# Kernel tuning notes

Measured on AMD Instinct MI355X. Metric: run time of the kernel, lower is better.

Reference implementation:

```python
import jax, jax.numpy as jnp
import numpy as np

R_MAX = 6.0
P = 3.0


def _envelope(distance, r_max=R_MAX, p=P):
    d = distance / r_max
    env = (1.0
           - (p + 1.0) * (p + 2.0) / 2.0 * d ** p
           + p * (p + 2.0) * d ** (p + 1.0)
           - p * (p + 1.0) / 2.0 * d ** (p + 2.0))
    return env * (distance < r_max)


def setup_inputs() -> dict:
    key = jax.random.key(0)
    k1, k2, k3, k4, k5 = jax.random.split(key, 5)
    N, K, C, SIZE = 50000, 32, 128, 128
    pair = jax.random.normal(k1, (N, K, C), dtype=jnp.float32)
    pair_update = jax.random.normal(k2, (N, K, SIZE), dtype=jnp.float32)
    neighbours = jax.random.randint(k3, (N, K), 0, N, dtype=jnp.int32)
    pair_mask = jnp.ones((N, K), dtype=bool)
    distance = jax.random.uniform(k4, (N,), dtype=jnp.float32)
    W = jax.random.normal(k5, (C, SIZE), dtype=jnp.float32) / np.sqrt(C)
    return {"pair": pair, "pair_update": pair_update, "neighbours": neighbours,
            "pair_mask": pair_mask, "distance": distance, "W": W}


def reference(pair, pair_update, neighbours, pair_mask, distance, W):
    N, K, _ = pair.shape
    size = W.shape[1]
    # gated message: sigmoid(pair @ W) * pair_update, shape [N, K, size]
    gate = jax.nn.sigmoid(jnp.einsum('nkc,cs->nks', pair, W))
    message = gate * pair_update
    message = jnp.where(pair_mask[..., None], message, 0)
    # polynomial envelope cutoff on per-node distance, broadcast [N,1,1]
    message = message * _envelope(distance)[:, None, None]
    # direction == 'outgoing': scatter-add over neighbour indices
    out = jnp.zeros((N, size), dtype=pair.dtype).at[neighbours].add(message)
    return out
```

## Files before the change

kernel.cpp:

```cpp
#include <hip/hip_runtime.h>
#include <stdint.h>

#define KNBR 32
#define CDIM 128
#define SDIM 128

typedef __bf16 bf16x8 __attribute__((ext_vector_type(8)));
typedef unsigned short ushortx8 __attribute__((ext_vector_type(8)));
typedef float f32x4 __attribute__((ext_vector_type(4)));

__device__ __forceinline__ unsigned short f32_bf16(float f) {
    unsigned int u = __builtin_bit_cast(unsigned int, f);
    u += 0x7FFFu + ((u >> 16) & 1u);
    return (unsigned short)(u >> 16);
}

__device__ __forceinline__ float envelope_fac(float dist, int msk) {
    const float d  = dist * (1.0f / 6.0f);
    const float d3 = d * d * d;
    float env = 1.0f - 10.0f * d3 + 15.0f * d3 * d - 6.0f * d3 * d * d;
    env = (dist < 6.0f) ? env : 0.0f;
    return (msk != 0) ? env : 0.0f;
}


__global__ void k_hist(const int* __restrict__ nbr, int* __restrict__ cnt, int np4) {
    const int i = blockIdx.x * blockDim.x + threadIdx.x;
    if (i < np4) {
        const int4 v = ((const int4*)nbr)[i];
        atomicAdd(&cnt[v.x], 1);
        atomicAdd(&cnt[v.y], 1);
        atomicAdd(&cnt[v.z], 1);
        atomicAdd(&cnt[v.w], 1);
    }
}

__global__ __launch_bounds__(256)
void k_blocksum(const int* __restrict__ cnt, int* __restrict__ bsum, int n) {
    const int t = threadIdx.x;
    const int e0 = blockIdx.x * 1024 + t * 4;
    int s = 0;
    if (e0 + 3 < n) {
        const int4 v = *(const int4*)(cnt + e0);
        s = v.x + v.y + v.z + v.w;
    } else {
        for (int j = 0; j < 4; ++j) if (e0 + j < n) s += cnt[e0 + j];
    }
#pragma unroll
    for (int off = 1; off < 64; off <<= 1) s += __shfl_xor(s, off);
    __shared__ int wt[4];
    if ((t & 63) == 0) wt[t >> 6] = s;
    __syncthreads();
    if (t == 0) bsum[blockIdx.x] = wt[0] + wt[1] + wt[2] + wt[3];
}

__global__ __launch_bounds__(1024)
void k_scanbsum(int* __restrict__ bsum, int nb) {
    __shared__ int lds[1024];
    const int t = threadIdx.x;
    const int own = (t < nb) ? bsum[t] : 0;
    lds[t] = own;
    __syncthreads();
    for (int off = 1; off < 1024; off <<= 1) {
        const int v = (t >= off) ? lds[t - off] : 0;
        __syncthreads();
        lds[t] += v;
        __syncthreads();
    }
    if (t < nb) bsum[t] = lds[t] - own;
}

__global__ __launch_bounds__(256)
void k_finalscan(const int* bsum, int* rowptr, int* cursor, int n) {
    const int t = threadIdx.x;
    const int e0 = blockIdx.x * 1024 + t * 4;
    int v[4] = {0, 0, 0, 0};
    if (e0 + 3 < n) {
        const int4 q = *(const int4*)(cursor + e0);
        v[0] = q.x; v[1] = q.y; v[2] = q.z; v[3] = q.w;
    } else {
        for (int j = 0; j < 4; ++j) if (e0 + j < n) v[j] = cursor[e0 + j];
    }
    const int s0 = v[0], s1 = s0 + v[1], s2 = s1 + v[2], s3 = s2 + v[3];
    const int lane = t & 63, wid = t >> 6;
    int incl = s3;
#pragma unroll
    for (int off = 1; off < 64; off <<= 1) {
        const int u = __shfl_up(incl, off);
        if (lane >= off) incl += u;
    }
    __shared__ int wt[4];
    if (lane == 63) wt[wid] = incl;
    __syncthreads();
    int wpre = 0;
    for (int w = 0; w < wid; ++w) wpre += wt[w];
    const int texcl = (incl - s3) + wpre + bsum[blockIdx.x];
    const int si[4] = {s0, s1, s2, s3};
    const int se[4] = {0, s0, s1, s2};
#pragma unroll
    for (int j = 0; j < 4; ++j) {
        const int e = e0 + j;
        if (e < n) {
            rowptr[1 + e] = texcl + si[j];
            cursor[e]     = texcl + se[j];
        }
    }
    if (blockIdx.x == 0 && t == 0) rowptr[0] = 0;
}

__global__ void k_scatter(const int* __restrict__ nbr, int* __restrict__ cursor,
                          int* __restrict__ elist, int np4) {
    const int i = blockIdx.x * blockDim.x + threadIdx.x;
    if (i < np4) {
        const int4 v = ((const int4*)nbr)[i];
        const int e0 = i * 4;
        elist[atomicAdd(&cursor[v.x], 1)] = e0;
        elist[atomicAdd(&cursor[v.y], 1)] = e0 + 1;
        elist[atomicAdd(&cursor[v.z], 1)] = e0 + 2;
        elist[atomicAdd(&cursor[v.w], 1)] = e0 + 3;
    }
}

__global__ __launch_bounds__(256, 3)
void k_gather(const float* __restrict__ pair,
              const float* __restrict__ pair_update,
              const int*   __restrict__ pair_mask,
              const float* __restrict__ distance,
              const float* __restrict__ W,
              const int*   __restrict__ rowptr,
              const int*   __restrict__ elist,
              float* __restrict__ out,
              int nnodes)
{
    __shared__ uint4 wlds[2048];
    const int tid  = threadIdx.x;
    const int lane = tid & 63;
    const int r16  = lane & 15;
    const int g    = lane >> 4;

    for (int e = tid; e < 2048; e += 256) {
        const int el = e & 63, kk = (e >> 6) & 3, ct = e >> 8;
        const int eg = el >> 4, er = el & 15;
        ushortx8 wb;
#pragma unroll
        for (int j = 0; j < 8; ++j)
            wb[j] = f32_bf16(W[(kk * 32 + eg * 8 + j) * SDIM + ct * 16 + er]);
        wlds[e] = __builtin_bit_cast(uint4, wb);
    }
    __syncthreads();

    const int wave   = (int)((blockIdx.x * blockDim.x + tid) >> 6);
    const int nwaves = (int)((gridDim.x * blockDim.x) >> 6);

    int wbase = 0;

    for (int n0 = wave; n0 < nnodes; n0 += nwaves) {
        const int n    = __builtin_amdgcn_readfirstlane(n0);
        const int base = rowptr[n];
        const int deg  = rowptr[n + 1] - base;
        const int ntile = (deg + 15) >> 4;

        float accs[8];
#pragma unroll
        for (int ct = 0; ct < 8; ++ct) accs[ct] = 0.0f;

        for (int t = 0; t < ntile; ++t) {
            const int slotA = t * 16 + r16;
            const int idxA  = base + ((slotA < deg) ? slotA : 0);
            const int emA   = elist[idxA];
            const float dA  = distance[emA >> 5];
            const int   mA  = pair_mask[emA];
            float facA = envelope_fac(dA, mA);
            facA = (slotA < deg) ? facA : 0.0f;

            int em_e[4]; float fac_e[4];
#pragma unroll
            for (int reg = 0; reg < 4; ++reg) {
                em_e[reg]  = __shfl(emA,  g * 4 + reg);
                fac_e[reg] = __shfl(facA, g * 4 + reg);
            }

            float puv[4][8];
#pragma unroll
            for (int reg = 0; reg < 4; ++reg) {
                const float* pub = pair_update + (size_t)em_e[reg] * SDIM + r16;
#pragma unroll
                for (int ct = 0; ct < 8; ++ct) puv[reg][ct] = pub[ct * 16];
            }

            const float* arow = pair + (size_t)emA * CDIM + g * 8;
            bf16x8 afrag[4];
#pragma unroll
            for (int kk = 0; kk < 4; ++kk) {
                const f32x4 v0 = *(const f32x4*)(arow + kk * 32);
                const f32x4 v1 = *(const f32x4*)(arow + kk * 32 + 4);
                ushortx8 ab;
#pragma unroll
                for (int j = 0; j < 4; ++j) ab[j] = f32_bf16(v0[j]);
#pragma unroll
                for (int j = 0; j < 4; ++j) ab[4 + j] = f32_bf16(v1[j]);
                afrag[kk] = __builtin_bit_cast(bf16x8, ab);
            }

            f32x4 acc[8];
#pragma unroll
            for (int ct = 0; ct < 8; ++ct) acc[ct] = (f32x4){0.f, 0.f, 0.f, 0.f};
            asm volatile("" : "+v"(wbase));
#pragma unroll
            for (int kk = 0; kk < 4; ++kk) {
#pragma unroll
                for (int ct = 0; ct < 8; ++ct) {
                    const uint4* wp = (const uint4*)((const char*)wlds + wbase)
                                      + (ct * 4 + kk) * 64 + lane;
                    const bf16x8 b = __builtin_bit_cast(bf16x8, *wp);
                    acc[ct] = __builtin_amdgcn_mfma_f32_16x16x32_bf16(
                        afrag[kk], b, acc[ct], 0, 0, 0);
                }
            }

#pragma unroll
            for (int reg = 0; reg < 4; ++reg) {
#pragma unroll
                for (int ct = 0; ct < 8; ++ct) {
                    const float logit = acc[ct][reg];
                    const float gate  = __builtin_amdgcn_rcpf(1.0f + __expf(-logit));
                    accs[ct] += gate * puv[reg][ct] * fac_e[reg];
                }
            }
        }

#pragma unroll
        for (int ct = 0; ct < 8; ++ct) {
            float v = accs[ct];
            v += __shfl_xor(v, 16);
            v += __shfl_xor(v, 32);
            accs[ct] = v;
        }
        float* orow = out + (size_t)n * SDIM;
        orow[lane]      = accs[g];
        orow[lane + 64] = accs[4 + g];
    }
}

__global__ __launch_bounds__(256, 2)
void orb_message_atomic(const float* __restrict__ pair,
                        const float* __restrict__ pair_update,
                        const int*   __restrict__ neighbours,
                        const int*   __restrict__ pair_mask,
                        const float* __restrict__ distance,
                        const float* __restrict__ W,
                        float* __restrict__ out,
                        int ntiles)
{
    const int lane = threadIdx.x & 63;
    const int r16  = lane & 15;
    const int g    = lane >> 4;
    const int wave   = (int)((blockIdx.x * blockDim.x + threadIdx.x) >> 6);
    const int nwaves = (int)((gridDim.x * blockDim.x) >> 6);

    bf16x8 wfrag[8][4];
#pragma unroll
    for (int ct = 0; ct < 8; ++ct)
#pragma unroll
        for (int kk = 0; kk < 4; ++kk) {
            ushortx8 wb;
#pragma unroll
            for (int j = 0; j < 8; ++j)
                wb[j] = f32_bf16(W[(kk * 32 + g * 8 + j) * SDIM + ct * 16 + r16]);
            wfrag[ct][kk] = __builtin_bit_cast(bf16x8, wb);
        }

    for (int t = wave; t < ntiles; t += nwaves) {
        const int p0 = t * 16;
        bf16x8 afrag[4];
        const float* arow = pair + (size_t)(p0 + r16) * CDIM + g * 8;
#pragma unroll
        for (int kk = 0; kk < 4; ++kk) {
            const f32x4 v0 = *(const f32x4*)(arow + kk * 32);
            const f32x4 v1 = *(const f32x4*)(arow + kk * 32 + 4);
            ushortx8 ab;
#pragma unroll
            for (int j = 0; j < 4; ++j) ab[j] = f32_bf16(v0[j]);
#pragma unroll
            for (int j = 0; j < 4; ++j) ab[4 + j] = f32_bf16(v1[j]);
            afrag[kk] = __builtin_bit_cast(bf16x8, ab);
        }
        f32x4 acc[8];
#pragma unroll
        for (int ct = 0; ct < 8; ++ct) acc[ct] = (f32x4){0.f, 0.f, 0.f, 0.f};
#pragma unroll
        for (int kk = 0; kk < 4; ++kk)
#pragma unroll
            for (int ct = 0; ct < 8; ++ct)
                acc[ct] = __builtin_amdgcn_mfma_f32_16x16x32_bf16(
                    afrag[kk], wfrag[ct][kk], acc[ct], 0, 0, 0);
#pragma unroll
        for (int reg = 0; reg < 4; ++reg) {
            const int p   = p0 + g * 4 + reg;
            const int tgt = neighbours[p];
            const float fac = envelope_fac(distance[p >> 5], pair_mask[p]);
            const float* pu = pair_update + (size_t)p * SDIM + r16;
            float* op = out + (size_t)tgt * SDIM + r16;
#pragma unroll
            for (int ct = 0; ct < 8; ++ct) {
                const float logit = acc[ct][reg];
                const float gate  = __builtin_amdgcn_rcpf(1.0f + __expf(-logit));
                unsafeAtomicAdd(op + ct * 16, gate * pu[ct * 16] * fac);
            }
        }
    }
}

extern "C" void kernel_launch(void* const* d_in, const int* in_sizes, int n_in,
                              void* d_out, int out_size, void* d_ws, size_t ws_size,
                              hipStream_t stream) {
    const float* pair        = (const float*)d_in[0];
    const float* pair_update = (const float*)d_in[1];
    const int*   neighbours  = (const int*)d_in[2];
    const int*   pair_mask   = (const int*)d_in[3];
    const float* distance    = (const float*)d_in[4];
    const float* W           = (const float*)d_in[5];
    float* out = (float*)d_out;

    const int N      = in_sizes[4];
    const int npairs = N * KNBR;
    const int nb     = (N + 1023) / 1024;

    const size_t need = ((size_t)N + (size_t)(N + 1) + (size_t)npairs + (size_t)nb)
                        * sizeof(int);
    if (ws_size < need || (npairs & 3) != 0 || nb > 1024) {
        hipMemsetAsync(d_out, 0, (size_t)out_size * sizeof(float), stream);
        orb_message_atomic<<<dim3(512), dim3(256), 0, stream>>>(
            pair, pair_update, neighbours, pair_mask, distance, W, out, npairs / 16);
        return;
    }

    int* cursor = (int*)d_ws;
    int* rowptr = cursor + N;
    int* elist  = rowptr + (N + 1);
    int* bsum   = elist + npairs;

    const int np4 = npairs / 4;

    hipMemsetAsync(cursor, 0, (size_t)N * sizeof(int), stream);
    k_hist     <<<dim3((np4 + 255) / 256), dim3(256),  0, stream>>>(neighbours, cursor, np4);
    k_blocksum <<<dim3(nb),                dim3(256),  0, stream>>>(cursor, bsum, N);
    k_scanbsum <<<dim3(1),                 dim3(1024), 0, stream>>>(bsum, nb);
    k_finalscan<<<dim3(nb),                dim3(256),  0, stream>>>(bsum, rowptr, cursor, N);
    k_scatter  <<<dim3((np4 + 255) / 256), dim3(256),  0, stream>>>(neighbours, cursor, elist, np4);
    k_gather   <<<dim3(4096),              dim3(256),  0, stream>>>(
        pair, pair_update, pair_mask, distance, W, rowptr, elist, out, N);
}
```

Baseline: 550.6 us.

## Precompute envelope factors in scatter and prefetch next tile's edge entries

The scatter pass now computes each pair's masked envelope factor and stores it with the edge id as an int2 in the edge list. This removes the dependent distance and mask loads from the gather kernel's inner loop. The gather loop also loads the next tile's edge entry one iteration early and issues the pair-row loads before the pair_update loads, to shorten the dependent load chain. The cost is a wider edge list, which doubles its write and read traffic, plus a few extra registers in the gather kernel.

```diff
diff --git a/kernel.cpp b/kernel.cpp
--- a/kernel.cpp
+++ b/kernel.cpp
@@ -108,27 +108,33 @@
     if (blockIdx.x == 0 && t == 0) rowptr[0] = 0;
 }
 
-__global__ void k_scatter(const int* __restrict__ nbr, int* __restrict__ cursor,
-                          int* __restrict__ elist, int np4) {
+__global__ void k_scatter(const int* __restrict__ nbr,
+                          const int* __restrict__ pair_mask,
+                          const float* __restrict__ distance,
+                          int* __restrict__ cursor,
+                          int2* __restrict__ elist2, int np4) {
     const int i = blockIdx.x * blockDim.x + threadIdx.x;
     if (i < np4) {
         const int4 v = ((const int4*)nbr)[i];
+        const int4 m = ((const int4*)pair_mask)[i];
         const int e0 = i * 4;
-        elist[atomicAdd(&cursor[v.x], 1)] = e0;
-        elist[atomicAdd(&cursor[v.y], 1)] = e0 + 1;
-        elist[atomicAdd(&cursor[v.z], 1)] = e0 + 2;
-        elist[atomicAdd(&cursor[v.w], 1)] = e0 + 3;
+        const float f0 = envelope_fac(distance[(e0 + 0) >> 5], m.x);
+        const float f1 = envelope_fac(distance[(e0 + 1) >> 5], m.y);
+        const float f2 = envelope_fac(distance[(e0 + 2) >> 5], m.z);
+        const float f3 = envelope_fac(distance[(e0 + 3) >> 5], m.w);
+        elist2[atomicAdd(&cursor[v.x], 1)] = make_int2(e0,     __builtin_bit_cast(int, f0));
+        elist2[atomicAdd(&cursor[v.y], 1)] = make_int2(e0 + 1, __builtin_bit_cast(int, f1));
+        elist2[atomicAdd(&cursor[v.z], 1)] = make_int2(e0 + 2, __builtin_bit_cast(int, f2));
+        elist2[atomicAdd(&cursor[v.w], 1)] = make_int2(e0 + 3, __builtin_bit_cast(int, f3));
     }
 }
 
 __global__ __launch_bounds__(256, 3)
 void k_gather(const float* __restrict__ pair,
               const float* __restrict__ pair_update,
-              const int*   __restrict__ pair_mask,
-              const float* __restrict__ distance,
               const float* __restrict__ W,
               const int*   __restrict__ rowptr,
-              const int*   __restrict__ elist,
+              const int2*  __restrict__ elist2,
               float* __restrict__ out,
               int nnodes)
 {
@@ -164,14 +170,20 @@
 #pragma unroll
         for (int ct = 0; ct < 8; ++ct) accs[ct] = 0.0f;
 
+        int emA = 0; float facA = 0.0f;
+        if (ntile > 0) {
+            const int slot = r16;
+            const int2 q = elist2[base + ((slot < deg) ? slot : 0)];
+            emA  = q.x;
+            facA = (slot < deg) ? __builtin_bit_cast(float, q.y) : 0.0f;
+        }
+
         for (int t = 0; t < ntile; ++t) {
-            const int slotA = t * 16 + r16;
-            const int idxA  = base + ((slotA < deg) ? slotA : 0);
-            const int emA   = elist[idxA];
-            const float dA  = distance[emA >> 5];
-            const int   mA  = pair_mask[emA];
-            float facA = envelope_fac(dA, mA);
-            facA = (slotA < deg) ? facA : 0.0f;
+            const int tn = (t + 1 < ntile) ? (t + 1) : t;
+            const int slotN = tn * 16 + r16;
+            const int2 qN = elist2[base + ((slotN < deg) ? slotN : 0)];
+            const int   emN  = qN.x;
+            const float facN = (slotN < deg) ? __builtin_bit_cast(float, qN.y) : 0.0f;
 
             int em_e[4]; float fac_e[4];
 #pragma unroll
@@ -180,6 +192,14 @@
                 fac_e[reg] = __shfl(facA, g * 4 + reg);
             }
 
+            const float* arow = pair + (size_t)emA * CDIM + g * 8;
+            f32x4 av[4][2];
+#pragma unroll
+            for (int kk = 0; kk < 4; ++kk) {
+                av[kk][0] = *(const f32x4*)(arow + kk * 32);
+                av[kk][1] = *(const f32x4*)(arow + kk * 32 + 4);
+            }
+
             float puv[4][8];
 #pragma unroll
             for (int reg = 0; reg < 4; ++reg) {
@@ -188,17 +208,14 @@
                 for (int ct = 0; ct < 8; ++ct) puv[reg][ct] = pub[ct * 16];
             }
 
-            const float* arow = pair + (size_t)emA * CDIM + g * 8;
             bf16x8 afrag[4];
 #pragma unroll
             for (int kk = 0; kk < 4; ++kk) {
-                const f32x4 v0 = *(const f32x4*)(arow + kk * 32);
-                const f32x4 v1 = *(const f32x4*)(arow + kk * 32 + 4);
                 ushortx8 ab;
 #pragma unroll
-                for (int j = 0; j < 4; ++j) ab[j] = f32_bf16(v0[j]);
-#pragma unroll
-                for (int j = 0; j < 4; ++j) ab[4 + j] = f32_bf16(v1[j]);
+                for (int j = 0; j < 4; ++j) ab[j]     = f32_bf16(av[kk][0][j]);
+#pragma unroll
+                for (int j = 0; j < 4; ++j) ab[4 + j] = f32_bf16(av[kk][1][j]);
                 afrag[kk] = __builtin_bit_cast(bf16x8, ab);
             }
 
@@ -227,6 +244,8 @@
                     accs[ct] += gate * puv[reg][ct] * fac_e[reg];
                 }
             }
+
+            emA = emN; facA = facN;
         }
 
 #pragma unroll
@@ -326,8 +345,8 @@
     const int npairs = N * KNBR;
     const int nb     = (N + 1023) / 1024;
 
-    const size_t need = ((size_t)N + (size_t)(N + 1) + (size_t)npairs + (size_t)nb)
-                        * sizeof(int);
+    const size_t need = (size_t)npairs * 8
+                      + ((size_t)N + (size_t)(N + 1) + (size_t)nb) * sizeof(int);
     if (ws_size < need || (npairs & 3) != 0 || nb > 1024) {
         hipMemsetAsync(d_out, 0, (size_t)out_size * sizeof(float), stream);
         orb_message_atomic<<<dim3(512), dim3(256), 0, stream>>>(
@@ -335,10 +354,10 @@
         return;
     }
 
-    int* cursor = (int*)d_ws;
-    int* rowptr = cursor + N;
-    int* elist  = rowptr + (N + 1);
-    int* bsum   = elist + npairs;
+    int2* elist2 = (int2*)d_ws;
+    int*  cursor = (int*)(elist2 + npairs);
+    int*  rowptr = cursor + N;
+    int*  bsum   = rowptr + (N + 1);
 
     const int np4 = npairs / 4;
 
@@ -347,7 +366,8 @@
     k_blocksum <<<dim3(nb),                dim3(256),  0, stream>>>(cursor, bsum, N);
     k_scanbsum <<<dim3(1),                 dim3(1024), 0, stream>>>(bsum, nb);
     k_finalscan<<<dim3(nb),                dim3(256),  0, stream>>>(bsum, rowptr, cursor, N);
-    k_scatter  <<<dim3((np4 + 255) / 256), dim3(256),  0, stream>>>(neighbours, cursor, elist, np4);
+    k_scatter  <<<dim3((np4 + 255) / 256), dim3(256),  0, stream>>>(
+        neighbours, pair_mask, distance, cursor, elist2, np4);
     k_gather   <<<dim3(4096),              dim3(256),  0, stream>>>(
-        pair, pair_update, pair_mask, distance, W, rowptr, elist, out, N);
-}
+        pair, pair_update, W, rowptr, elist2, out, N);
+}
```

Result: no change. 547.9 us (-0.5%).
